# Optimization experiments

Hardware: AMD Instinct MI355X
Metric: run time of the kernel (lower is better)

## Reference

```python
import jax, jax.numpy as jnp
import numpy as np

B, N, NODE_DIM, COND_DIM, EDGE_DIM = 16, 256, 512, 512, 128
E_TOT = 262144  # total edges, divisible by B
EPS = 1e-5


def weight_norm(v, g):
    # torch weight_norm dim=0: per-output-row normalization. v: [out, in], g: [out]
    return v * (g / jnp.sqrt(jnp.sum(v * v, axis=1)))[:, None]


def setup_inputs() -> dict:
    key = jax.random.key(0)
    ks = jax.random.split(key, 12)
    node_feats = jax.random.normal(ks[0], (B, N, NODE_DIM), dtype=jnp.float32)
    cond_feats = jax.random.normal(ks[1], (B, COND_DIM), dtype=jnp.float32)
    edge_indexes = jnp.sort(jax.random.randint(ks[2], (E_TOT,), 0, B * N * N, dtype=jnp.int64))
    s_node = 1.0 / np.sqrt(NODE_DIM)
    s_cond = 1.0 / np.sqrt(COND_DIM)
    s_film = 1.0 / np.sqrt(2 * EDGE_DIM)
    return {
        "node_feats": node_feats,
        "cond_feats": cond_feats,
        "edge_indexes": edge_indexes,
        "v_node": jax.random.uniform(ks[3], (EDGE_DIM, NODE_DIM), jnp.float32, -s_node, s_node),
        "g_node": jnp.ones((EDGE_DIM,), jnp.float32),
        "b_node": jnp.zeros((EDGE_DIM,), jnp.float32),
        "v_cond": jax.random.uniform(ks[4], (2 * EDGE_DIM, COND_DIM), jnp.float32, -s_cond, s_cond),
        "g_cond": jnp.ones((2 * EDGE_DIM,), jnp.float32),
        "b_cond": jnp.zeros((2 * EDGE_DIM,), jnp.float32),
        "w_film": jax.random.uniform(ks[5], (EDGE_DIM, 2 * EDGE_DIM), jnp.float32, -s_film, s_film),
        "b_film": jnp.zeros((EDGE_DIM,), jnp.float32),
    }


def reference(node_feats, cond_feats, edge_indexes, v_node, g_node, b_node,
              v_cond, g_cond, b_cond, w_film, b_film):
    # node projection: Dropout(0) -> weight_norm Linear -> ReLU
    w_n = weight_norm(v_node, g_node)
    nodes = jax.nn.relu(jnp.einsum('bnd,ed->bne', node_feats, w_n) + b_node)  # [B,N,E]

    # cond projection -> gamma, beta
    w_c = weight_norm(v_cond, g_cond)
    gb = cond_feats @ w_c.T + b_cond  # [B, 2E]
    gamma = gb[:, :EDGE_DIM] + 1.0
    beta = gb[:, EDGE_DIM:]

    # gather edge endpoints directly (equivalent to materializing [B,N,N,2E] 'cat' then indexing)
    b_idx = edge_indexes // (N * N)
    i_idx = (edge_indexes // N) % N
    j_idx = edge_indexes % N
    fused = jnp.concatenate([nodes[b_idx, i_idx], nodes[b_idx, j_idx]], axis=-1)  # [E_TOT, 2E]

    # film_l: linear -> LayerNorm(no affine) -> FiLM -> ReLU, on view (B, E_TOT//B, E)
    x = fused @ w_film.T + b_film  # [E_TOT, EDGE_DIM]
    x = x.reshape(B, E_TOT // B, EDGE_DIM)
    mu = jnp.mean(x, axis=-1, keepdims=True)
    var = jnp.mean(jnp.square(x - mu), axis=-1, keepdims=True)
    x = (x - mu) * jax.lax.rsqrt(var + EPS)
    x = x * gamma[:, None, :] + beta[:, None, :]
    x = jax.nn.relu(x)
    return x.reshape(E_TOT, EDGE_DIM)
```

## Files before the change

### kernel.cpp

```cpp
#include <hip/hip_runtime.h>
#include <hip/hip_bf16.h>

typedef __bf16 bf16_t;
typedef bf16_t bf16x8 __attribute__((ext_vector_type(8)));
typedef bf16_t bf16x4 __attribute__((ext_vector_type(4)));
typedef float f32x4 __attribute__((ext_vector_type(4)));

#define NODE_DIM 512
#define COND_DIM 512
#define EDGE_DIM 128

#define WS_WN   0x000000
#define WS_WC   0x020000
#define WS_SC   0x030000
#define WS_GA   0x031000
#define WS_BE   0x033000
#define WS_P    0x040000

__device__ __forceinline__ bf16x8 cvt8(float4 a, float4 b) {
    bf16x8 v;
    v[0] = (bf16_t)a.x; v[1] = (bf16_t)a.y; v[2] = (bf16_t)a.z; v[3] = (bf16_t)a.w;
    v[4] = (bf16_t)b.x; v[5] = (bf16_t)b.y; v[6] = (bf16_t)b.z; v[7] = (bf16_t)b.w;
    return v;
}

__global__ __launch_bounds__(256) void prep_kernel(
    const float* __restrict__ cond_feats,
    const float* __restrict__ v_node, const float* __restrict__ g_node,
    const float* __restrict__ v_cond, const float* __restrict__ g_cond,
    const float* __restrict__ b_cond, const float* __restrict__ w_film,
    char* __restrict__ ws)
{
    bf16_t* Wn = (bf16_t*)(ws + WS_WN);
    bf16_t* Wc = (bf16_t*)(ws + WS_WC);
    float* scale_node = (float*)(ws + WS_SC);
    float* gamma = (float*)(ws + WS_GA);
    float* beta  = (float*)(ws + WS_BE);

    int t = threadIdx.x;
    int bid = blockIdx.x;
    int lane = t & 63, wv = t >> 6;

    if (bid < 32) {
        size_t idx = ((size_t)bid * 256 + t) * 8;
        float4 a = ((const float4*)(v_node + idx))[0];
        float4 b = ((const float4*)(v_node + idx))[1];
        *(bf16x8*)(Wn + idx) = cvt8(a, b);
    } else if (bid < 48) {
        int u = (bid - 32) * 256 + t;
        int n = u >> 4;
        int ko = (u & 15) * 8;
        const float* src = (n < 128) ? (w_film + (size_t)n * 256 + ko)
                                     : (w_film + (size_t)(n - 128) * 256 + 128 + ko);
        float4 a = ((const float4*)src)[0];
        float4 b = ((const float4*)src)[1];
        *(bf16x8*)(Wc + (size_t)n * 128 + ko) = cvt8(a, b);
    } else if (bid < 80) {
        int id = (bid - 48) * 4 + wv;
        const float* vn = v_node + (size_t)id * NODE_DIM + lane * 8;
        float sq = 0.f;
#pragma unroll
        for (int i = 0; i < 2; i++) {
            float4 v4 = ((const float4*)vn)[i];
            sq += v4.x * v4.x + v4.y * v4.y + v4.z * v4.z + v4.w * v4.w;
        }
#pragma unroll
        for (int o = 32; o > 0; o >>= 1) sq += __shfl_xor(sq, o);
        if (lane == 0) scale_node[id] = g_node[id] * rsqrtf(sq);
    } else {
        int id = (bid - 80) * 4 + wv;
        int b = id >> 8, n = id & 255;
        const float* cf = cond_feats + b * COND_DIM + lane * 8;
        const float* vc = v_cond + (size_t)n * COND_DIM + lane * 8;
        float dot = 0.f, sq = 0.f;
#pragma unroll
        for (int i = 0; i < 2; i++) {
            float4 c4 = ((const float4*)cf)[i];
            float4 v4 = ((const float4*)vc)[i];
            dot += c4.x * v4.x + c4.y * v4.y + c4.z * v4.z + c4.w * v4.w;
            sq  += v4.x * v4.x + v4.y * v4.y + v4.z * v4.z + v4.w * v4.w;
        }
#pragma unroll
        for (int o = 32; o > 0; o >>= 1) {
            dot += __shfl_xor(dot, o);
            sq  += __shfl_xor(sq, o);
        }
        if (lane == 0) {
            float val = dot * (g_cond[n] * rsqrtf(sq)) + b_cond[n];
            if (n < 128) gamma[b * 128 + n] = val + 1.0f;
            else         beta[b * 128 + (n - 128)] = val;
        }
    }
}

__global__ __launch_bounds__(256) void gemm_kernel(
    const float* __restrict__ node_feats, const float* __restrict__ b_node,
    char* __restrict__ ws)
{
    const bf16_t* Wn = (const bf16_t*)(ws + WS_WN);
    const bf16_t* Wc = (const bf16_t*)(ws + WS_WC);
    const float* scale_node = (const float*)(ws + WS_SC);
    bf16_t* P = (bf16_t*)(ws + WS_P);

    __shared__ __attribute__((aligned(16))) bf16_t N_s[16 * 136];
    __shared__ __attribute__((aligned(16))) float  T_s[4][16][68];

    int t = threadIdx.x;
    int lane = t & 63, w = t >> 6;
    int r16 = lane & 15, half = lane >> 4;
    int m0 = blockIdx.x * 16;

    f32x4 zero4 = {0.f, 0.f, 0.f, 0.f};

    f32x4 acc0 = zero4, acc1 = zero4;
    {
        const float*  aptr = node_feats + (size_t)(m0 + r16) * NODE_DIM + half * 8;
        const bf16_t* bptr = Wn + (size_t)(w * 32 + r16) * NODE_DIM + half * 8;
#pragma unroll
        for (int ks = 0; ks < 16; ks++) {
            float4 a0 = ((const float4*)(aptr + ks * 32))[0];
            float4 a1 = ((const float4*)(aptr + ks * 32))[1];
            bf16x8 af = cvt8(a0, a1);
            bf16x8 b0 = *(const bf16x8*)(bptr + ks * 32);
            bf16x8 b1 = *(const bf16x8*)(bptr + 16 * NODE_DIM + ks * 32);
            acc0 = __builtin_amdgcn_mfma_f32_16x16x32_bf16(af, b0, acc0, 0, 0, 0);
            acc1 = __builtin_amdgcn_mfma_f32_16x16x32_bf16(af, b1, acc1, 0, 0, 0);
        }
    }
    {
        int rbase = half * 4;
#pragma unroll
        for (int j = 0; j < 2; j++) {
            int col = w * 32 + j * 16 + r16;
            float s = scale_node[col], bb = b_node[col];
            f32x4 a = j ? acc1 : acc0;
#pragma unroll
            for (int r = 0; r < 4; r++) {
                float v = fmaxf(a[r] * s + bb, 0.f);
                N_s[(rbase + r) * 136 + col] = (bf16_t)v;
            }
        }
    }
    __syncthreads();

    f32x4 acc2[4];
#pragma unroll
    for (int i = 0; i < 4; i++) acc2[i] = zero4;
    {
        const bf16_t* bptr = Wc + (size_t)(w * 64 + r16) * 128 + half * 8;
#pragma unroll
        for (int ks = 0; ks < 4; ks++) {
            bf16x8 af = *(const bf16x8*)&N_s[r16 * 136 + ks * 32 + half * 8];
#pragma unroll
            for (int j = 0; j < 4; j++) {
                bf16x8 bf = *(const bf16x8*)(bptr + j * 16 * 128 + ks * 32);
                acc2[j] = __builtin_amdgcn_mfma_f32_16x16x32_bf16(af, bf, acc2[j], 0, 0, 0);
            }
        }
    }
    {
        int rbase = half * 4;
#pragma unroll
        for (int j = 0; j < 4; j++) {
            int col = j * 16 + r16;
#pragma unroll
            for (int r = 0; r < 4; r++) T_s[w][rbase + r][col] = acc2[j][r];
        }
    }
    __syncthreads();
    {
#pragma unroll
        for (int r2 = 0; r2 < 2; r2++) {
            int row = r2 * 8 + (lane >> 3);
            int colg = (lane & 7) * 8;
            float4 a = *(const float4*)&T_s[w][row][colg];
            float4 b = *(const float4*)&T_s[w][row][colg + 4];
            *(bf16x8*)&P[(size_t)(m0 + row) * 256 + w * 64 + colg] = cvt8(a, b);
        }
    }
}

__global__ __launch_bounds__(256) void edge_kernel(
    const int* __restrict__ edges, const char* __restrict__ ws,
    const float* __restrict__ b_film, float* __restrict__ out)
{
    const bf16_t* P = (const bf16_t*)(ws + WS_P);
    const float* gamma = (const float*)(ws + WS_GA);
    const float* beta  = (const float*)(ws + WS_BE);

    int t = threadIdx.x;
    int l16  = t & 15;
    int rsub = t >> 4;
    int c = l16 * 8;

    int base = (blockIdx.x & 7) * 32768 + (blockIdx.x >> 3) * 32;
    int bb = base >> 14;

    float4 g0  = *(const float4*)&gamma[bb * 128 + c];
    float4 g1  = *(const float4*)&gamma[bb * 128 + c + 4];
    float4 be0 = *(const float4*)&beta[bb * 128 + c];
    float4 be1 = *(const float4*)&beta[bb * 128 + c + 4];
    float4 bf0 = *(const float4*)&b_film[c];
    float4 bf1 = *(const float4*)&b_film[c + 4];

#pragma unroll
    for (int it = 0; it < 2; it++) {
        int r = base + it * 16 + rsub;
        int e = edges[r];
        int ri = e >> 8;
        int rj = ((e >> 16) << 8) | (e & 255);

        bf16x8 p1 = *(const bf16x8*)&P[(size_t)ri * 256 + c];
        bf16x8 p2 = *(const bf16x8*)&P[(size_t)rj * 256 + 128 + c];

        float x0 = (float)p1[0] + (float)p2[0] + bf0.x;
        float x1 = (float)p1[1] + (float)p2[1] + bf0.y;
        float x2 = (float)p1[2] + (float)p2[2] + bf0.z;
        float x3 = (float)p1[3] + (float)p2[3] + bf0.w;
        float x4 = (float)p1[4] + (float)p2[4] + bf1.x;
        float x5 = (float)p1[5] + (float)p2[5] + bf1.y;
        float x6 = (float)p1[6] + (float)p2[6] + bf1.z;
        float x7 = (float)p1[7] + (float)p2[7] + bf1.w;

        float s  = ((x0 + x1) + (x2 + x3)) + ((x4 + x5) + (x6 + x7));
        float ss = x0 * x0 + x1 * x1 + x2 * x2 + x3 * x3
                 + x4 * x4 + x5 * x5 + x6 * x6 + x7 * x7;
#pragma unroll
        for (int m = 8; m >= 1; m >>= 1) {
            s  += __shfl_xor(s, m);
            ss += __shfl_xor(ss, m);
        }
        float mu  = s * (1.0f / 128.0f);
        float var = ss * (1.0f / 128.0f) - mu * mu;
        float rs  = rsqrtf(var + 1e-5f);

        f32x4 o0, o1;
        o0[0] = fmaxf((x0 - mu) * rs * g0.x + be0.x, 0.f);
        o0[1] = fmaxf((x1 - mu) * rs * g0.y + be0.y, 0.f);
        o0[2] = fmaxf((x2 - mu) * rs * g0.z + be0.z, 0.f);
        o0[3] = fmaxf((x3 - mu) * rs * g0.w + be0.w, 0.f);
        o1[0] = fmaxf((x4 - mu) * rs * g1.x + be1.x, 0.f);
        o1[1] = fmaxf((x5 - mu) * rs * g1.y + be1.y, 0.f);
        o1[2] = fmaxf((x6 - mu) * rs * g1.z + be1.z, 0.f);
        o1[3] = fmaxf((x7 - mu) * rs * g1.w + be1.w, 0.f);

        __builtin_nontemporal_store(o0, (f32x4*)&out[(size_t)r * 128 + c]);
        __builtin_nontemporal_store(o1, (f32x4*)&out[(size_t)r * 128 + c + 4]);
    }
}

extern "C" void kernel_launch(void* const* d_in, const int* in_sizes, int n_in,
                              void* d_out, int out_size, void* d_ws, size_t ws_size,
                              hipStream_t stream) {
    const float* node_feats = (const float*)d_in[0];
    const float* cond_feats = (const float*)d_in[1];
    const int*   edges      = (const int*)d_in[2];
    const float* v_node     = (const float*)d_in[3];
    const float* g_node     = (const float*)d_in[4];
    const float* b_node     = (const float*)d_in[5];
    const float* v_cond     = (const float*)d_in[6];
    const float* g_cond     = (const float*)d_in[7];
    const float* b_cond     = (const float*)d_in[8];
    const float* w_film     = (const float*)d_in[9];
    const float* b_film     = (const float*)d_in[10];
    float* out = (float*)d_out;
    char* ws = (char*)d_ws;

    prep_kernel<<<1104, 256, 0, stream>>>(cond_feats, v_node, g_node,
                                          v_cond, g_cond, b_cond, w_film, ws);
    gemm_kernel<<<256, 256, 0, stream>>>(node_feats, b_node, ws);
    edge_kernel<<<8192, 256, 0, stream>>>(edges, ws, b_film, out);
}
```

Baseline: 190.9 us.

## Fuse prep and node GEMM kernels, convert weights to bf16 inline

Merges the weight-prep kernel and the node/film GEMM kernel into one launch. Blocks below 256 do the GEMMs, reading fp32 v_node and w_film directly and converting them to bf16 in registers; they also compute the weight-norm row scale on the fly. The remaining 1024 blocks compute gamma/beta. This removes one kernel launch, the intermediate bf16 weight buffers and a dependency barrier. The cost is redundant fp32 weight loads and sum-of-squares work repeated in every GEMM block.

```diff
diff --git a/kernel.cpp b/kernel.cpp
--- a/kernel.cpp
+++ b/kernel.cpp
@@ -3,19 +3,14 @@
 
 typedef __bf16 bf16_t;
 typedef bf16_t bf16x8 __attribute__((ext_vector_type(8)));
-typedef bf16_t bf16x4 __attribute__((ext_vector_type(4)));
 typedef float f32x4 __attribute__((ext_vector_type(4)));
 
 #define NODE_DIM 512
 #define COND_DIM 512
-#define EDGE_DIM 128
-
-#define WS_WN   0x000000
-#define WS_WC   0x020000
-#define WS_SC   0x030000
-#define WS_GA   0x031000
-#define WS_BE   0x033000
-#define WS_P    0x040000
+
+#define WS_GA   0x000000
+#define WS_BE   0x002000
+#define WS_P    0x010000
 
 __device__ __forceinline__ bf16x8 cvt8(float4 a, float4 b) {
     bf16x8 v;
@@ -24,51 +19,22 @@
     return v;
 }
 
-__global__ __launch_bounds__(256) void prep_kernel(
-    const float* __restrict__ cond_feats,
+__global__ __launch_bounds__(256) void fused_kernel(
+    const float* __restrict__ node_feats, const float* __restrict__ cond_feats,
     const float* __restrict__ v_node, const float* __restrict__ g_node,
-    const float* __restrict__ v_cond, const float* __restrict__ g_cond,
-    const float* __restrict__ b_cond, const float* __restrict__ w_film,
-    char* __restrict__ ws)
+    const float* __restrict__ b_node, const float* __restrict__ v_cond,
+    const float* __restrict__ g_cond, const float* __restrict__ b_cond,
+    const float* __restrict__ w_film, char* __restrict__ ws)
 {
-    bf16_t* Wn = (bf16_t*)(ws + WS_WN);
-    bf16_t* Wc = (bf16_t*)(ws + WS_WC);
-    float* scale_node = (float*)(ws + WS_SC);
     float* gamma = (float*)(ws + WS_GA);
     float* beta  = (float*)(ws + WS_BE);
+    bf16_t* P = (bf16_t*)(ws + WS_P);
 
     int t = threadIdx.x;
-    int bid = blockIdx.x;
-    int lane = t & 63, wv = t >> 6;
-
-    if (bid < 32) {
-        size_t idx = ((size_t)bid * 256 + t) * 8;
-        float4 a = ((const float4*)(v_node + idx))[0];
-        float4 b = ((const float4*)(v_node + idx))[1];
-        *(bf16x8*)(Wn + idx) = cvt8(a, b);
-    } else if (bid < 48) {
-        int u = (bid - 32) * 256 + t;
-        int n = u >> 4;
-        int ko = (u & 15) * 8;
-        const float* src = (n < 128) ? (w_film + (size_t)n * 256 + ko)
-                                     : (w_film + (size_t)(n - 128) * 256 + 128 + ko);
-        float4 a = ((const float4*)src)[0];
-        float4 b = ((const float4*)src)[1];
-        *(bf16x8*)(Wc + (size_t)n * 128 + ko) = cvt8(a, b);
-    } else if (bid < 80) {
-        int id = (bid - 48) * 4 + wv;
-        const float* vn = v_node + (size_t)id * NODE_DIM + lane * 8;
-        float sq = 0.f;
-#pragma unroll
-        for (int i = 0; i < 2; i++) {
-            float4 v4 = ((const float4*)vn)[i];
-            sq += v4.x * v4.x + v4.y * v4.y + v4.z * v4.z + v4.w * v4.w;
-        }
-#pragma unroll
-        for (int o = 32; o > 0; o >>= 1) sq += __shfl_xor(sq, o);
-        if (lane == 0) scale_node[id] = g_node[id] * rsqrtf(sq);
-    } else {
-        int id = (bid - 80) * 4 + wv;
+    int lane = t & 63, w = t >> 6;
+
+    if (blockIdx.x >= 256) {
+        int id = ((int)blockIdx.x - 256) * 4 + w;
         int b = id >> 8, n = id & 255;
         const float* cf = cond_feats + b * COND_DIM + lane * 8;
         const float* vc = v_cond + (size_t)n * COND_DIM + lane * 8;
@@ -90,49 +56,50 @@
             if (n < 128) gamma[b * 128 + n] = val + 1.0f;
             else         beta[b * 128 + (n - 128)] = val;
         }
-    }
-}
-
-__global__ __launch_bounds__(256) void gemm_kernel(
-    const float* __restrict__ node_feats, const float* __restrict__ b_node,
-    char* __restrict__ ws)
-{
-    const bf16_t* Wn = (const bf16_t*)(ws + WS_WN);
-    const bf16_t* Wc = (const bf16_t*)(ws + WS_WC);
-    const float* scale_node = (const float*)(ws + WS_SC);
-    bf16_t* P = (bf16_t*)(ws + WS_P);
+        return;
+    }
 
     __shared__ __attribute__((aligned(16))) bf16_t N_s[16 * 136];
     __shared__ __attribute__((aligned(16))) float  T_s[4][16][68];
 
-    int t = threadIdx.x;
-    int lane = t & 63, w = t >> 6;
     int r16 = lane & 15, half = lane >> 4;
     int m0 = blockIdx.x * 16;
 
     f32x4 zero4 = {0.f, 0.f, 0.f, 0.f};
 
     f32x4 acc0 = zero4, acc1 = zero4;
-    {
-        const float*  aptr = node_feats + (size_t)(m0 + r16) * NODE_DIM + half * 8;
-        const bf16_t* bptr = Wn + (size_t)(w * 32 + r16) * NODE_DIM + half * 8;
+    float sq0 = 0.f, sq1 = 0.f;
+    {
+        const float* aptr = node_feats + (size_t)(m0 + r16) * NODE_DIM + half * 8;
+        const float* b0p  = v_node + (size_t)(w * 32 + r16) * NODE_DIM + half * 8;
+        const float* b1p  = b0p + 16 * NODE_DIM;
 #pragma unroll
         for (int ks = 0; ks < 16; ks++) {
             float4 a0 = ((const float4*)(aptr + ks * 32))[0];
             float4 a1 = ((const float4*)(aptr + ks * 32))[1];
+            float4 c0 = ((const float4*)(b0p + ks * 32))[0];
+            float4 c1 = ((const float4*)(b0p + ks * 32))[1];
+            float4 d0 = ((const float4*)(b1p + ks * 32))[0];
+            float4 d1 = ((const float4*)(b1p + ks * 32))[1];
+            sq0 += c0.x*c0.x + c0.y*c0.y + c0.z*c0.z + c0.w*c0.w
+                 + c1.x*c1.x + c1.y*c1.y + c1.z*c1.z + c1.w*c1.w;
+            sq1 += d0.x*d0.x + d0.y*d0.y + d0.z*d0.z + d0.w*d0.w
+                 + d1.x*d1.x + d1.y*d1.y + d1.z*d1.z + d1.w*d1.w;
             bf16x8 af = cvt8(a0, a1);
-            bf16x8 b0 = *(const bf16x8*)(bptr + ks * 32);
-            bf16x8 b1 = *(const bf16x8*)(bptr + 16 * NODE_DIM + ks * 32);
-            acc0 = __builtin_amdgcn_mfma_f32_16x16x32_bf16(af, b0, acc0, 0, 0, 0);
-            acc1 = __builtin_amdgcn_mfma_f32_16x16x32_bf16(af, b1, acc1, 0, 0, 0);
-        }
-    }
+            acc0 = __builtin_amdgcn_mfma_f32_16x16x32_bf16(af, cvt8(c0, c1), acc0, 0, 0, 0);
+            acc1 = __builtin_amdgcn_mfma_f32_16x16x32_bf16(af, cvt8(d0, d1), acc1, 0, 0, 0);
+        }
+    }
+    sq0 += __shfl_xor(sq0, 16); sq0 += __shfl_xor(sq0, 32);
+    sq1 += __shfl_xor(sq1, 16); sq1 += __shfl_xor(sq1, 32);
+
     {
         int rbase = half * 4;
 #pragma unroll
         for (int j = 0; j < 2; j++) {
             int col = w * 32 + j * 16 + r16;
-            float s = scale_node[col], bb = b_node[col];
+            float s = g_node[col] * rsqrtf(j ? sq1 : sq0);
+            float bb = b_node[col];
             f32x4 a = j ? acc1 : acc0;
 #pragma unroll
             for (int r = 0; r < 4; r++) {
@@ -147,14 +114,21 @@
 #pragma unroll
     for (int i = 0; i < 4; i++) acc2[i] = zero4;
     {
-        const bf16_t* bptr = Wc + (size_t)(w * 64 + r16) * 128 + half * 8;
+        const float* wsrc[4];
+#pragma unroll
+        for (int j = 0; j < 4; j++) {
+            int n = w * 64 + j * 16 + r16;
+            wsrc[j] = (n < 128) ? (w_film + (size_t)n * 256 + half * 8)
+                                : (w_film + (size_t)(n - 128) * 256 + 128 + half * 8);
+        }
 #pragma unroll
         for (int ks = 0; ks < 4; ks++) {
             bf16x8 af = *(const bf16x8*)&N_s[r16 * 136 + ks * 32 + half * 8];
 #pragma unroll
             for (int j = 0; j < 4; j++) {
-                bf16x8 bf = *(const bf16x8*)(bptr + j * 16 * 128 + ks * 32);
-                acc2[j] = __builtin_amdgcn_mfma_f32_16x16x32_bf16(af, bf, acc2[j], 0, 0, 0);
+                float4 e0 = ((const float4*)(wsrc[j] + ks * 32))[0];
+                float4 e1 = ((const float4*)(wsrc[j] + ks * 32))[1];
+                acc2[j] = __builtin_amdgcn_mfma_f32_16x16x32_bf16(af, cvt8(e0, e1), acc2[j], 0, 0, 0);
             }
         }
     }
@@ -266,8 +240,7 @@
     float* out = (float*)d_out;
     char* ws = (char*)d_ws;
 
-    prep_kernel<<<1104, 256, 0, stream>>>(cond_feats, v_node, g_node,
-                                          v_cond, g_cond, b_cond, w_film, ws);
-    gemm_kernel<<<256, 256, 0, stream>>>(node_feats, b_node, ws);
+    fused_kernel<<<1280, 256, 0, stream>>>(node_feats, cond_feats, v_node, g_node,
+                                           b_node, v_cond, g_cond, b_cond, w_film, ws);
     edge_kernel<<<8192, 256, 0, stream>>>(edges, ws, b_film, out);
 }
```

Result: slower. 202.7 us (+6.2%).
